# Optimization experiments

Hardware: AMD Instinct MI355X
Metric: run time of the kernel (lower is better)

The kernel has to match this reference:

```python
import jax, jax.numpy as jnp
import numpy as np


def _lsa(cost):
    """Jonker-Volgenant shortest-augmenting-path linear sum assignment.
    cost: [n, n] numpy float64, rows = ground_truth, cols = prediction.
    Returns col_of_row: col_of_row[i] = column assigned to row i.
    Matches scipy.optimize.linear_sum_assignment on square matrices."""
    n = cost.shape[0]
    INF = np.inf
    u = np.zeros(n + 1)
    v = np.zeros(n + 1)
    p = np.zeros(n + 1, dtype=np.int64)   # p[j] = row matched to column j (1-indexed, 0 = none)
    way = np.zeros(n + 1, dtype=np.int64)
    for i in range(1, n + 1):
        p[0] = i
        j0 = 0
        minv = np.full(n + 1, INF)
        used = np.zeros(n + 1, dtype=bool)
        while True:
            used[j0] = True
            i0 = p[j0]
            free = ~used[1:]
            cur = cost[i0 - 1, :] - u[i0] - v[1:]
            upd = free & (cur < minv[1:])
            minv1 = minv[1:]
            way1 = way[1:]
            minv1[upd] = cur[upd]
            way1[upd] = j0
            masked = np.where(free, minv1, INF)
            j1 = int(np.argmin(masked)) + 1
            delta = masked[j1 - 1]
            u[p[used]] += delta
            v[used] -= delta
            minv[1:][free] -= delta
            j0 = j1
            if p[j0] == 0:
                break
        while True:
            j1 = way[j0]
            p[j0] = p[j1]
            j0 = j1
            if j0 == 0:
                break
    col_of_row = np.zeros(n, dtype=np.int64)
    for j in range(1, n + 1):
        col_of_row[p[j] - 1] = j - 1
    return col_of_row


def _hungarian_perms(pred_np, target_np):
    """Per-batch L1 cost matrices (rows=target, cols=pred) + assignment.
    Returns perms [B, N]: perms[b, i] = pred index matched to target point i."""
    # [B, N, N] L1 cdist, computed in float64 on host (faithful to scipy CPU path)
    cost = np.abs(target_np[:, :, None, :].astype(np.float64)
                  - pred_np[:, None, :, :].astype(np.float64)).sum(-1)
    return np.stack([_lsa(c) for c in cost], axis=0)


def setup_inputs() -> dict:
    key = jax.random.key(0)
    k1, k2 = jax.random.split(key)
    B, N = 128, 64
    pred = jax.random.uniform(k1, (B, N, 2), dtype=jnp.float32)
    target = jax.random.uniform(k2, (B, N, 2), dtype=jnp.float32)
    return {"pred": pred, "target": target}


def reference(pred, target):
    # Host-side Hungarian matching (mirrors the scipy CPU round-trip; indices
    # are data-dependent and non-differentiable, exactly as in the original).
    pred_np = np.asarray(jax.device_get(pred))
    target_np = np.asarray(jax.device_get(target))
    perms = jnp.asarray(_hungarian_perms(pred_np, target_np))  # [B, N] int

    # Gather matched predictions: pred_sorted[b, i] = pred[b, perms[b, i]]
    pred_sorted = jnp.take_along_axis(pred, perms[:, :, None], axis=1)
    # Per-batch F.l1_loss is a mean over N*2 elements; summing over batch and
    # dividing by B equals the global mean (all batch elements same size).
    return jnp.mean(jnp.abs(pred_sorted - target))
```

## Files before the change

### kernel.cpp

```cpp
#include <hip/hip_runtime.h>

#define BATCH 128
#define NPTS  64

template<int CTRL>
__device__ __forceinline__ int dpp_mov_i(int x) {
    return __builtin_amdgcn_update_dpp(x, x, CTRL, 0xF, 0xF, false);
}

__device__ __forceinline__ int imin(int a, int b) { return a < b ? a : b; }

__device__ __forceinline__ unsigned sadu(unsigned a, unsigned b, unsigned c) {
    return (a > b ? a - b : b - a) + c;
}

__global__ __launch_bounds__(64) void hungarian_kernel(
    const float* __restrict__ pred,
    const float* __restrict__ target,
    double* __restrict__ batch_cost)
{
    const int b    = blockIdx.x;
    const int lane = threadIdx.x;

    const float2 pr = ((const float2*)pred)[b * NPTS + lane];
    const float2 tg = ((const float2*)target)[b * NPTS + lane];
    const int pxi = (int)(pr.x * 8388608.0f);
    const int pyi = (int)(pr.y * 8388608.0f);
    const int txi = (int)(tg.x * 8388608.0f);
    const int tyi = (int)(tg.y * 8388608.0f);

    int vi  = 0;
    int cu  = 0;
    int ctx = 0, cty = 0;
    int pvx = pxi;
    unsigned long long freemask = ~0ull;

    for (int i = 0; i < NPTS; ++i) {
        const int rix = __builtin_amdgcn_readlane(txi, i);
        const int riy = __builtin_amdgcn_readlane(tyi, i);
        int key = (int)sadu((unsigned)rix, (unsigned)pvx,
                            sadu((unsigned)riy, (unsigned)pyi, 0u)) - vi;
        int  D = 0, Dsnap = 0, u0 = 0;
        bool sel = false;
        int  jf;

        for (;;) {
            int m  = key;
            int a1 = dpp_mov_i<0x111>(m);
            int a2 = dpp_mov_i<0x112>(m);
            m = imin(imin(m, a1), a2);
            a1 = dpp_mov_i<0x113>(m);
            a2 = dpp_mov_i<0x116>(m);
            m = imin(imin(m, a1), a2);
            a1 = dpp_mov_i<0x117>(m);
            m = imin(m, a1);
            int g = imin(imin(__builtin_amdgcn_readlane(m, 15),
                              __builtin_amdgcn_readlane(m, 31)),
                         imin(__builtin_amdgcn_readlane(m, 47),
                              __builtin_amdgcn_readlane(m, 63)));
            unsigned long long msk = __ballot(key == g);
            int j = __ffsll(msk) - 1;

            D += g - u0;
            bool me = (lane == j);
            if (me) Dsnap = D;

            if (freemask & (1ull << j)) { jf = j; break; }

            if (me) { pvx = 0x40000000; sel = true; }
            u0 = __builtin_amdgcn_readlane(cu, j);
            int ox = __builtin_amdgcn_readlane(ctx, j);
            int oy = __builtin_amdgcn_readlane(cty, j);
            key = (int)sadu((unsigned)ox, (unsigned)pvx,
                            sadu((unsigned)oy, (unsigned)pyi, 0u)) - vi;
        }

        int S = D - Dsnap;
        if (sel) { cu += S; vi -= S; pvx = pxi; }
        if (lane == jf) { ctx = rix; cty = riy; cu = D; }
        freemask &= ~(1ull << jf);
    }

    int ci = (int)sadu((unsigned)ctx, (unsigned)pxi,
                       sadu((unsigned)cty, (unsigned)pyi, 0u));
    #pragma unroll
    for (int s = 32; s >= 1; s >>= 1) ci += __shfl_xor(ci, s);
    if (lane == 0) batch_cost[b] = (double)ci * 0x1p-23;
}

__global__ __launch_bounds__(64) void reduce_kernel(
    const double* __restrict__ batch_cost,
    float* __restrict__ out)
{
    int t = threadIdx.x;
    double x = batch_cost[t] + batch_cost[t + 64];
    #pragma unroll
    for (int s = 32; s >= 1; s >>= 1) x += __shfl_xor(x, s);
    if (t == 0) out[0] = (float)(x / (double)(BATCH * NPTS * 2));
}

extern "C" void kernel_launch(void* const* d_in, const int* in_sizes, int n_in,
                              void* d_out, int out_size, void* d_ws, size_t ws_size,
                              hipStream_t stream)
{
    const float* pred   = (const float*)d_in[0];
    const float* target = (const float*)d_in[1];
    double* batch_cost  = (double*)d_ws;

    hungarian_kernel<<<BATCH, 64, 0, stream>>>(pred, target, batch_cost);
    reduce_kernel<<<1, 64, 0, stream>>>(batch_cost, (float*)d_out);
}
```

Baseline: 59.45 us.

## Pack lane index into min-key, drop ballot, fuse reduction via atomics

The Hungarian inner loop now packs the column index into the low 6 bits of the reduced cost key, so the wave-wide min gives both value and argmin. This removes the ballot/ffs step, and used columns are masked with a max sentinel instead of a large coordinate. The separate reduce kernel is replaced by an atomic accumulate plus a last-block-done counter, with a memset to clear the accumulator. The tradeoffs are reduced integer headroom for costs (shift by 6), a memset launch and atomic contention.

```diff
diff --git a/kernel.cpp b/kernel.cpp
--- a/kernel.cpp
+++ b/kernel.cpp
@@ -9,6 +9,7 @@
 }
 
 __device__ __forceinline__ int imin(int a, int b) { return a < b ? a : b; }
+__device__ __forceinline__ int imax(int a, int b) { return a > b ? a : b; }
 
 __device__ __forceinline__ unsigned sadu(unsigned a, unsigned b, unsigned c) {
     return (a > b ? a - b : b - a) + c;
@@ -17,7 +18,8 @@
 __global__ __launch_bounds__(64) void hungarian_kernel(
     const float* __restrict__ pred,
     const float* __restrict__ target,
-    double* __restrict__ batch_cost)
+    unsigned long long* __restrict__ acc,
+    float* __restrict__ out)
 {
     const int b    = blockIdx.x;
     const int lane = threadIdx.x;
@@ -29,20 +31,22 @@
     const int txi = (int)(tg.x * 8388608.0f);
     const int tyi = (int)(tg.y * 8388608.0f);
 
-    int vi  = 0;
+    int v6  = 0;
     int cu  = 0;
     int ctx = 0, cty = 0;
-    int pvx = pxi;
     unsigned long long freemask = ~0ull;
 
     for (int i = 0; i < NPTS; ++i) {
         const int rix = __builtin_amdgcn_readlane(txi, i);
         const int riy = __builtin_amdgcn_readlane(tyi, i);
-        int key = (int)sadu((unsigned)rix, (unsigned)pvx,
-                            sadu((unsigned)riy, (unsigned)pyi, 0u)) - vi;
-        int  D = 0, Dsnap = 0, u0 = 0;
-        bool sel = false;
-        int  jf;
+        const int base = lane - v6;
+
+        int c0  = (int)sadu((unsigned)rix, (unsigned)pxi,
+                            sadu((unsigned)riy, (unsigned)pyi, 0u));
+        int key = (int)(((unsigned)c0 << 6) + (unsigned)base);
+        int selbig = (int)0x80000000;
+        int D = 0, Dsnap = 0, u0 = 0;
+        int jf;
 
         for (;;) {
             int m  = key;
@@ -58,25 +62,27 @@
                               __builtin_amdgcn_readlane(m, 31)),
                          imin(__builtin_amdgcn_readlane(m, 47),
                               __builtin_amdgcn_readlane(m, 63)));
-            unsigned long long msk = __ballot(key == g);
-            int j = __ffsll(msk) - 1;
 
-            D += g - u0;
+            int j = g & 63;
+            D += (g >> 6) - u0;
             bool me = (lane == j);
             if (me) Dsnap = D;
 
-            if (freemask & (1ull << j)) { jf = j; break; }
+            int u0n = __builtin_amdgcn_readlane(cu,  j);
+            int ox  = __builtin_amdgcn_readlane(ctx, j);
+            int oy  = __builtin_amdgcn_readlane(cty, j);
 
-            if (me) { pvx = 0x40000000; sel = true; }
-            u0 = __builtin_amdgcn_readlane(cu, j);
-            int ox = __builtin_amdgcn_readlane(ctx, j);
-            int oy = __builtin_amdgcn_readlane(cty, j);
-            key = (int)sadu((unsigned)ox, (unsigned)pvx,
-                            sadu((unsigned)oy, (unsigned)pyi, 0u)) - vi;
+            if ((freemask >> j) & 1ull) { jf = j; break; }
+
+            if (me) selbig = 0x7FFFFFFF;
+            u0 = u0n;
+            int c2 = (int)sadu((unsigned)ox, (unsigned)pxi,
+                               sadu((unsigned)oy, (unsigned)pyi, 0u));
+            key = imax((int)(((unsigned)c2 << 6) + (unsigned)base), selbig);
         }
 
         int S = D - Dsnap;
-        if (sel) { cu += S; vi -= S; pvx = pxi; }
+        if (selbig == 0x7FFFFFFF) { cu += S; v6 -= (S << 6); }
         if (lane == jf) { ctx = rix; cty = riy; cu = D; }
         freemask &= ~(1ull << jf);
     }
@@ -85,18 +91,17 @@
                        sadu((unsigned)cty, (unsigned)pyi, 0u));
     #pragma unroll
     for (int s = 32; s >= 1; s >>= 1) ci += __shfl_xor(ci, s);
-    if (lane == 0) batch_cost[b] = (double)ci * 0x1p-23;
-}
 
-__global__ __launch_bounds__(64) void reduce_kernel(
-    const double* __restrict__ batch_cost,
-    float* __restrict__ out)
-{
-    int t = threadIdx.x;
-    double x = batch_cost[t] + batch_cost[t + 64];
-    #pragma unroll
-    for (int s = 32; s >= 1; s >>= 1) x += __shfl_xor(x, s);
-    if (t == 0) out[0] = (float)(x / (double)(BATCH * NPTS * 2));
+    if (lane == 0) {
+        atomicAdd(acc, (unsigned long long)(unsigned)ci);
+        __threadfence();
+        unsigned old = atomicAdd((unsigned*)(acc + 1), 1u);
+        if (old == BATCH - 1) {
+            __threadfence();
+            unsigned long long tot = atomicAdd(acc, 0ull);
+            out[0] = (float)((double)tot * 0x1p-23 / (double)(BATCH * NPTS * 2));
+        }
+    }
 }
 
 extern "C" void kernel_launch(void* const* d_in, const int* in_sizes, int n_in,
@@ -105,8 +110,8 @@
 {
     const float* pred   = (const float*)d_in[0];
     const float* target = (const float*)d_in[1];
-    double* batch_cost  = (double*)d_ws;
+    unsigned long long* acc = (unsigned long long*)d_ws;
 
-    hungarian_kernel<<<BATCH, 64, 0, stream>>>(pred, target, batch_cost);
-    reduce_kernel<<<1, 64, 0, stream>>>(batch_cost, (float*)d_out);
+    hipMemsetAsync(acc, 0, 16, stream);
+    hungarian_kernel<<<BATCH, 64, 0, stream>>>(pred, target, acc, (float*)d_out);
 }
```

Measured after the change: 57.25 us. 3.7% less time.
